# Kernel tuning notes

Measured on AMD Instinct MI355X. Metric: run time of the kernel, lower is better.

## Reference

```python
import jax, jax.numpy as jnp
import numpy as np

N, E, NREL = 50000, 800000, 4
IN, EMB, HID, OUT, LVL = 32, 32, 32, 32, 3


def setup_inputs() -> dict:
    key = jax.random.key(0)
    ks = jax.random.split(key, 24)
    f32 = jnp.float32
    inp = {
        'x': jax.random.normal(ks[0], (N, IN), f32),
        'node_feat': jax.random.normal(ks[1], (N, EMB), f32),
        'edge_feat': jax.random.normal(ks[2], (E, EMB), f32),
        'src': jax.random.randint(ks[3], (E,), 0, N, jnp.int32),
        'dst': jax.random.randint(ks[4], (E,), 0, N, jnp.int32),
        'eid': jax.random.randint(ks[5], (E,), 0, NREL, jnp.int32),
        # layer 1 (in_feat=IN)
        'Wr1': jax.random.normal(ks[6], (NREL, IN + 2 * EMB, HID), f32) * 0.1,
        'attn_w1': jax.random.normal(ks[7], (EMB + HID, 1), f32) * 0.1,
        'loop_w1': jax.random.normal(ks[8], (EMB, HID), f32) * 0.1,
        'h_bias1': jax.random.normal(ks[9], (HID,), f32) * 0.1,
        'amrm_W1': jax.random.normal(ks[10], (LVL, HID, HID), f32) * 0.1,
        'amrm_b1': jax.random.normal(ks[11], (LVL, HID), f32) * 0.1,
        'amrm_a1': jax.random.normal(ks[12], (HID, 1), f32) * 0.1,
        # layer 2 (in_feat=HID)
        'Wr2': jax.random.normal(ks[13], (NREL, HID + 2 * EMB, OUT), f32) * 0.1,
        'attn_w2': jax.random.normal(ks[14], (EMB + OUT, 1), f32) * 0.1,
        'loop_w2': jax.random.normal(ks[15], (EMB, OUT), f32) * 0.1,
        'h_bias2': jax.random.normal(ks[16], (OUT,), f32) * 0.1,
        'amrm_W2': jax.random.normal(ks[17], (LVL, OUT, OUT), f32) * 0.1,
        'amrm_b2': jax.random.normal(ks[18], (LVL, OUT), f32) * 0.1,
        'amrm_a2': jax.random.normal(ks[19], (OUT, 1), f32) * 0.1,
    }
    return inp


def _rp_layer(feat, node_feat, src, dst, eid, edge_feat,
              Wr, attn_w, loop_w, h_bias, amrm_W, amrm_b, amrm_a):
    n = node_feat.shape[0]
    ones_e = jnp.ones((src.shape[0],), feat.dtype)
    # symmetric-ish degree norm: feat scaled by out-degree^-1/2
    deg_out = jnp.clip(jax.ops.segment_sum(ones_e, src, num_segments=n), 1.0)
    feat = feat * (deg_out ** -0.5)[:, None]
    # per-edge gather + relation-typed linear (grouped GEMM over NREL types)
    xe = jnp.concatenate([feat[src], edge_feat, node_feat[dst]], axis=1)  # [E, in+2*emb]
    m = jnp.zeros((xe.shape[0], Wr.shape[2]), feat.dtype)
    for r in range(Wr.shape[0]):
        m = m + jnp.where((eid == r)[:, None], xe @ Wr[r], 0.0)
    # edge attention + segment softmax over incoming edges per dst node
    z = jax.nn.leaky_relu(jnp.concatenate([node_feat[dst], m], axis=1) @ attn_w)  # [E,1]
    zmax = jax.ops.segment_max(z, dst, num_segments=n)
    ez = jnp.exp(z - zmax[dst])
    a = ez / jax.ops.segment_sum(ez, dst, num_segments=n)[dst]
    # scatter-sum aggregation
    h = jax.ops.segment_sum(a * m, dst, num_segments=n)
    h = h + node_feat @ loop_w
    deg_in = jnp.clip(jax.ops.segment_sum(ones_e, dst, num_segments=n), 1.0)
    h = h * (deg_in ** -0.5)[:, None] + h_bias
    # adaptive multi-level relation module
    lv = jax.nn.relu(jnp.einsum('nh,lho->nlo', h, amrm_W) + amrm_b[None])  # [N,L,O]
    sc = jax.nn.softmax(jnp.einsum('nlo,o->nl', lv, amrm_a[:, 0]), axis=-1)  # [N,L]
    return jnp.einsum('nl,nlo->no', sc, lv)


def reference(x, node_feat, edge_feat, src, dst, eid,
              Wr1, attn_w1, loop_w1, h_bias1, amrm_W1, amrm_b1, amrm_a1,
              Wr2, attn_w2, loop_w2, h_bias2, amrm_W2, amrm_b2, amrm_a2):
    h = jax.nn.relu(_rp_layer(x, node_feat, src, dst, eid, edge_feat,
                              Wr1, attn_w1, loop_w1, h_bias1, amrm_W1, amrm_b1, amrm_a1))
    h = jax.nn.relu(_rp_layer(h, node_feat, src, dst, eid, edge_feat,
                              Wr2, attn_w2, loop_w2, h_bias2, amrm_W2, amrm_b2, amrm_a2))
    return h
```

## Files before the change

### kernel.cpp

```cpp
#include <hip/hip_runtime.h>

#define NN 50000
#define NE 800000

#define O_DEGIN   0
#define O_DEGOUT  50048
#define O_ROWPTR  100096
#define O_CURSOR  150208
#define O_EINFO   200256
#define O_FEATN   1800256
#define O_ZF      3400256
#define O_ZNRD    3600320
#define O_VV      3800384
#define O_EZ      3800832
#define O_NFT     4600832
#define O_WDENT   6200832
#define O_YACC    6450880
#define O_H1      19250880
#define O_WT      20850880


__global__ __launch_bounds__(256) void k_deg(const int* __restrict__ src,
                                             const int* __restrict__ dst,
                                             int* degin, int* degout) {
    int e = blockIdx.x * 256 + threadIdx.x;
    if (e < NE) {
        atomicAdd(&degin[dst[e]], 1);
        atomicAdd(&degout[src[e]], 1);
    }
}

__global__ __launch_bounds__(1024) void k_scan(const int* __restrict__ degin,
                                               int* rowptr, int* cursor) {
    __shared__ int swsum[16];
    __shared__ int stot;
    int t = threadIdx.x;
    int lane = t & 63, w = t >> 6;
    int carry = 0;
    for (int ch = 0; ch < 4; ch++) {
        int base = ch * 16384 + t * 16;
        int v[16];
        int s = 0;
#pragma unroll
        for (int j = 0; j < 16; j++) {
            v[j] = (base + j < NN) ? degin[base + j] : 0;
            s += v[j];
        }
        int incl = s;
#pragma unroll
        for (int off = 1; off < 64; off <<= 1) {
            int x = __shfl_up(incl, off, 64);
            if (lane >= off) incl += x;
        }
        if (lane == 63) swsum[w] = incl;
        __syncthreads();
        if (w == 0) {
            int y = (lane < 16) ? swsum[lane] : 0;
            int yi = y;
#pragma unroll
            for (int off = 1; off < 16; off <<= 1) {
                int x = __shfl_up(yi, off, 64);
                if (lane >= off) yi += x;
            }
            if (lane < 16) swsum[lane] = yi - y;
            if (lane == 15) stot = yi;
        }
        __syncthreads();
        int excl = carry + swsum[w] + (incl - s);
#pragma unroll
        for (int j = 0; j < 16; j++) {
            if (base + j < NN) { rowptr[base + j] = excl; cursor[base + j] = excl; }
            excl += v[j];
        }
        carry += stot;
        __syncthreads();
    }
    if (t == 0) rowptr[NN] = carry;
}

__global__ __launch_bounds__(256) void k_scatter(const int* __restrict__ src,
                                                 const int* __restrict__ dst,
                                                 const int* __restrict__ eid,
                                                 int* cursor, int2* einfo) {
    int e = blockIdx.x * 256 + threadIdx.x;
    if (e >= NE) return;
    int slot = atomicAdd(&cursor[dst[e]], 1);
    einfo[slot] = make_int2(src[e] | (eid[e] << 20), e);
}


__global__ __launch_bounds__(384) void k_prevec(const float* __restrict__ Wr,
                                                const float* __restrict__ attw,
                                                float* __restrict__ vvec) {
    int t = threadIdx.x;
    int r = (t >> 5) & 3, k = t & 31, part = t >> 7;
    int row = (part == 0) ? (32 + k) : (part == 1) ? k : (64 + k);
    const float* wrow = Wr + (size_t)r * 3072 + row * 32;
    float s = 0.f;
#pragma unroll
    for (int c = 0; c < 32; c++) s += wrow[c] * attw[32 + c];
    vvec[t] = s;
}

__global__ __launch_bounds__(512) void k_wt(const float* __restrict__ Wr,
                                            const float* __restrict__ lw,
                                            const float* __restrict__ aW,
                                            float* __restrict__ WT) {
    int tid = threadIdx.x;
    int mat = tid >> 5, i = tid & 31;
    const float* srcb;
    if (mat < 4)        srcb = Wr + (size_t)mat * 3072 + i;
    else if (mat < 8)   srcb = Wr + (size_t)(mat - 4) * 3072 + 1024 + i;
    else if (mat < 12)  srcb = Wr + (size_t)(mat - 8) * 3072 + 2048 + i;
    else if (mat == 12) srcb = lw + i;
    else                srcb = aW + (size_t)(mat - 13) * 1024 + i;
    float* d = WT + (size_t)mat * 1024 + (size_t)i * 4;
#pragma unroll
    for (int c = 0; c < 32; c++)
        d[(c >> 2) * 128 + (c & 3)] = srcb[(size_t)c * 32];
}

__global__ __launch_bounds__(128) void k_nodeproj(const float* __restrict__ feat,
                                                  const float* __restrict__ nfeat,
                                                  const float* __restrict__ attw,
                                                  const float* __restrict__ vvec,
                                                  const int* __restrict__ degout,
                                                  float* __restrict__ featn,
                                                  float* __restrict__ nfT,
                                                  float* __restrict__ zF,
                                                  float* __restrict__ znrd) {
    int n = blockIdx.x * 128 + threadIdx.x;
    if (n >= NN) return;
    int dg = degout[n];
    float sc0 = rsqrtf((float)(dg > 1 ? dg : 1));
    const float* fin = feat + (size_t)n * 32;
    const float* nin = nfeat + (size_t)n * 32;
    float fv[32], nv[32];
#pragma unroll
    for (int k = 0; k < 32; k += 4) {
        float4 f4 = *(const float4*)&fin[k];
        fv[k] = f4.x * sc0; fv[k + 1] = f4.y * sc0;
        fv[k + 2] = f4.z * sc0; fv[k + 3] = f4.w * sc0;
        float4 n4 = *(const float4*)&nin[k];
        nv[k] = n4.x; nv[k + 1] = n4.y; nv[k + 2] = n4.z; nv[k + 3] = n4.w;
    }
    float* fo = featn + (size_t)n * 32;
#pragma unroll
    for (int k = 0; k < 32; k += 4)
        *(float4*)&fo[k] = make_float4(fv[k], fv[k + 1], fv[k + 2], fv[k + 3]);
#pragma unroll
    for (int k = 0; k < 32; k++) nfT[(size_t)k * NN + n] = nv[k];
    float zn = 0.f;
#pragma unroll
    for (int k = 0; k < 32; k++) zn += nv[k] * attw[k];
#pragma unroll
    for (int r = 0; r < 4; r++) {
        float zf = 0.f, zd = 0.f;
        const float* vf = vvec + 128 + r * 32;
        const float* vd = vvec + 256 + r * 32;
#pragma unroll
        for (int k = 0; k < 32; k++) { zf += fv[k] * vf[k]; zd += nv[k] * vd[k]; }
        zF[r * NN + n] = zf;
        znrd[r * NN + n] = zn + zd;
    }
}

__global__ __launch_bounds__(256) void k_ez(const int* __restrict__ src,
                                            const int* __restrict__ dst,
                                            const int* __restrict__ eid,
                                            const float* __restrict__ efeat,
                                            const float* __restrict__ zF,
                                            const float* __restrict__ znrd,
                                            const float* __restrict__ vvec,
                                            float* __restrict__ ez) {
    int e = blockIdx.x * 256 + threadIdx.x;
    int s = src[e], d = dst[e], r = eid[e];
    const float* er = efeat + (size_t)e * 32;
    float d0 = 0.f, d1 = 0.f, d2 = 0.f, d3 = 0.f;
#pragma unroll
    for (int k = 0; k < 32; k += 4) {
        float4 f = *(const float4*)&er[k];
        d0 += f.x * vvec[k]       + f.y * vvec[k + 1]
            + f.z * vvec[k + 2]   + f.w * vvec[k + 3];
        d1 += f.x * vvec[32 + k]  + f.y * vvec[33 + k]
            + f.z * vvec[34 + k]  + f.w * vvec[35 + k];
        d2 += f.x * vvec[64 + k]  + f.y * vvec[65 + k]
            + f.z * vvec[66 + k]  + f.w * vvec[67 + k];
        d3 += f.x * vvec[96 + k]  + f.y * vvec[97 + k]
            + f.z * vvec[98 + k]  + f.w * vvec[99 + k];
    }
    float dot = (r == 0) ? d0 : (r == 1) ? d1 : (r == 2) ? d2 : d3;
    float z = znrd[r * NN + d] + zF[r * NN + s] + dot;
    z = z > 0.f ? z : 0.01f * z;
    ez[e] = __expf(z);
}

__global__ __launch_bounds__(512) void k_agg(const int* __restrict__ rowptr,
                                             const int2* __restrict__ einfo,
                                             const float* __restrict__ ez,
                                             const float* __restrict__ efeat,
                                             const float* __restrict__ featn,
                                             float* __restrict__ yacc,
                                             float* __restrict__ wdenT) {
    int tid = threadIdx.x;
    int lane = tid & 63;
    int wid = tid >> 6;
    int n0 = blockIdx.x * 8;
    int n = n0 + wid;
    int c = lane & 31;
    int p = lane >> 5;

    int rp0 = rowptr[n];
    int deg = rowptr[n + 1] - rp0;

    float yf0 = 0.f, yf1 = 0.f, yf2 = 0.f, yf3 = 0.f;
    float ye0 = 0.f, ye1 = 0.f, ye2 = 0.f, ye3 = 0.f;
    float w0 = 0.f, w1 = 0.f, w2 = 0.f, w3 = 0.f, den = 0.f;

    int2 meA = make_int2(0, 0), meB = make_int2(0, 0);
    float ezA = 0.f, efA = 0.f, fnA = 0.f;
    if (p < deg) {
        meA = einfo[rp0 + p];
        ezA = ez[meA.y];
        efA = efeat[(size_t)meA.y * 32 + c];
        fnA = featn[(size_t)(meA.x & 0xFFFFF) * 32 + c];
    }
    if (p + 2 < deg) meB = einfo[rp0 + p + 2];

    for (int t = p; t < deg; t += 2) {
        float ezB = 0.f, efB = 0.f, fnB = 0.f;
        int2 meC = make_int2(0, 0);
        if (t + 2 < deg) {
            ezB = ez[meB.y];
            efB = efeat[(size_t)meB.y * 32 + c];
            fnB = featn[(size_t)(meB.x & 0xFFFFF) * 32 + c];
        }
        if (t + 4 < deg) meC = einfo[rp0 + t + 4];
        int rb = meA.x >> 20;
        float e0 = (rb == 0) ? ezA : 0.f;
        float e1 = (rb == 1) ? ezA : 0.f;
        float e2 = (rb == 2) ? ezA : 0.f;
        float e3 = (rb == 3) ? ezA : 0.f;
        yf0 += e0 * fnA; yf1 += e1 * fnA; yf2 += e2 * fnA; yf3 += e3 * fnA;
        ye0 += e0 * efA; ye1 += e1 * efA; ye2 += e2 * efA; ye3 += e3 * efA;
        w0 += e0; w1 += e1; w2 += e2; w3 += e3;
        den += ezA;
        meA = meB; ezA = ezB; efA = efB; fnA = fnB; meB = meC;
    }

    yf0 += __shfl_xor(yf0, 32); yf1 += __shfl_xor(yf1, 32);
    yf2 += __shfl_xor(yf2, 32); yf3 += __shfl_xor(yf3, 32);
    ye0 += __shfl_xor(ye0, 32); ye1 += __shfl_xor(ye1, 32);
    ye2 += __shfl_xor(ye2, 32); ye3 += __shfl_xor(ye3, 32);
    w0 += __shfl_xor(w0, 32); w1 += __shfl_xor(w1, 32);
    w2 += __shfl_xor(w2, 32); w3 += __shfl_xor(w3, 32);
    den += __shfl_xor(den, 32);

    if (lane < 5) {
        float wv = (lane == 0) ? w0 : (lane == 1) ? w1 : (lane == 2) ? w2
                 : (lane == 3) ? w3 : den;
        wdenT[lane * NN + n] = wv;
    }

    float* yr = yacc + (size_t)n * 256 + p * 128 + c;
    yr[0]  = p ? ye0 : yf0;
    yr[32] = p ? ye1 : yf1;
    yr[64] = p ? ye2 : yf2;
    yr[96] = p ? ye3 : yf3;
}

__global__ __launch_bounds__(256) void k_postAB(const int* __restrict__ rowptr,
                                                const float* __restrict__ yacc,
                                                const float* __restrict__ wdenT,
                                                const float* __restrict__ nfeat,
                                                const float* __restrict__ WT,
                                                const float* __restrict__ hbias,
                                                const float* __restrict__ ab,
                                                const float* __restrict__ aa,
                                                float* __restrict__ out) {
    __shared__ alignas(16) float sy[8 * 256];
    __shared__ alignas(16) float snf[8 * 32];
    __shared__ float sh[8 * 32];
    int tid = threadIdx.x;
    int n0 = blockIdx.x * 8;

    {
        const float4* ys = (const float4*)(yacc + (size_t)n0 * 256);
        float4* yd = (float4*)sy;
        yd[tid] = ys[tid];
        yd[tid + 256] = ys[tid + 256];
        snf[tid] = nfeat[(size_t)n0 * 32 + tid];
    }
    __syncthreads();

    int lane = tid & 63;
    int wid = tid >> 6;
    int g = lane >> 5, i = lane & 31;
    int node = wid * 2 + g;
    int n = n0 + node;
    int deg = rowptr[n + 1] - rowptr[n];
    const float* row = sy + node * 256;
    const float* nv = snf + node * 32;
    const float* Wt = WT + (size_t)i * 4;

    float h = 0.f;
#pragma unroll 2
    for (int pr = 0; pr < 8; pr++) {
        const float* W = Wt + pr * 1024;
        const float* rw = row + pr * 32;
        float t = 0.f;
#pragma unroll
        for (int c = 0; c < 32; c += 4) {
            float4 wv = *(const float4*)&W[c * 32];
            float4 v  = *(const float4*)&rw[c];
            t += v.x * wv.x + v.y * wv.y + v.z * wv.z + v.w * wv.w;
        }
        h += t;
    }
#pragma unroll 1
    for (int r = 0; r < 4; r++) {
        float wr = wdenT[(size_t)r * NN + n];
        const float* W = Wt + (8 + r) * 1024;
        float t = 0.f;
#pragma unroll
        for (int c = 0; c < 32; c += 4) {
            float4 wv = *(const float4*)&W[c * 32];
            float4 v  = *(const float4*)&nv[c];
            t += v.x * wv.x + v.y * wv.y + v.z * wv.z + v.w * wv.w;
        }
        h += wr * t;
    }
    float den = wdenT[(size_t)4 * NN + n];
    h *= (deg > 0) ? 1.f / den : 0.f;
    {
        const float* W = Wt + 12 * 1024;
        float t = 0.f;
#pragma unroll
        for (int c = 0; c < 32; c += 4) {
            float4 wv = *(const float4*)&W[c * 32];
            float4 v  = *(const float4*)&nv[c];
            t += v.x * wv.x + v.y * wv.y + v.z * wv.z + v.w * wv.w;
        }
        h += t;
    }
    float hsc = rsqrtf((float)(deg > 1 ? deg : 1));
    h = h * hsc + hbias[i];
    sh[node * 32 + i] = h;

    const float* hn = sh + node * 32;
    float a0 = ab[i], a1 = ab[32 + i], a2 = ab[64 + i];
#pragma unroll 2
    for (int c = 0; c < 32; c += 4) {
        float4 v  = *(const float4*)&hn[c];
        float4 w0 = *(const float4*)&Wt[13 * 1024 + c * 32];
        float4 w1 = *(const float4*)&Wt[14 * 1024 + c * 32];
        float4 w2 = *(const float4*)&Wt[15 * 1024 + c * 32];
        a0 += v.x * w0.x + v.y * w0.y + v.z * w0.z + v.w * w0.w;
        a1 += v.x * w1.x + v.y * w1.y + v.z * w1.z + v.w * w1.w;
        a2 += v.x * w2.x + v.y * w2.y + v.z * w2.z + v.w * w2.w;
    }
    float lv0 = a0 > 0.f ? a0 : 0.f;
    float lv1 = a1 > 0.f ? a1 : 0.f;
    float lv2 = a2 > 0.f ? a2 : 0.f;
    float aai = aa[i];
    float s0 = lv0 * aai, s1 = lv1 * aai, s2 = lv2 * aai;
#pragma unroll
    for (int off = 16; off >= 1; off >>= 1) {
        s0 += __shfl_xor(s0, off);
        s1 += __shfl_xor(s1, off);
        s2 += __shfl_xor(s2, off);
    }
    float mx = fmaxf(s0, fmaxf(s1, s2));
    float e0 = __expf(s0 - mx), e1 = __expf(s1 - mx), e2 = __expf(s2 - mx);
    float inv = 1.f / (e0 + e1 + e2);
    float o = (e0 * lv0 + e1 * lv1 + e2 * lv2) * inv;
    out[(size_t)n * 32 + i] = fmaxf(o, 0.f);
}


static void launch_layer(const float* feat, const float* nf, const float* efeat,
                         const int* src, const int* dst, const int* eid,
                         const float* Wr, const float* attw, const float* lw,
                         const float* hb, const float* aW, const float* ab,
                         const float* aa, float* wsf, int* wsi, float* out,
                         hipStream_t stream) {
    k_prevec<<<1, 384, 0, stream>>>(Wr, attw, wsf + O_VV);
    k_wt<<<1, 512, 0, stream>>>(Wr, lw, aW, wsf + O_WT);
    k_nodeproj<<<391, 128, 0, stream>>>(feat, nf, attw, wsf + O_VV, wsi + O_DEGOUT,
                                        wsf + O_FEATN, wsf + O_NFT,
                                        wsf + O_ZF, wsf + O_ZNRD);
    k_ez<<<3125, 256, 0, stream>>>(src, dst, eid, efeat, wsf + O_ZF, wsf + O_ZNRD,
                                   wsf + O_VV, wsf + O_EZ);
    k_agg<<<6250, 512, 0, stream>>>(wsi + O_ROWPTR, (const int2*)(wsi + O_EINFO),
                                    wsf + O_EZ, efeat, wsf + O_FEATN,
                                    wsf + O_YACC, wsf + O_WDENT);
    k_postAB<<<6250, 256, 0, stream>>>(wsi + O_ROWPTR, wsf + O_YACC, wsf + O_WDENT,
                                       nf, wsf + O_WT, hb, ab, aa, out);
}

extern "C" void kernel_launch(void* const* d_in, const int* in_sizes, int n_in,
                              void* d_out, int out_size, void* d_ws, size_t ws_size,
                              hipStream_t stream) {
    const float* x     = (const float*)d_in[0];
    const float* nfeat = (const float*)d_in[1];
    const float* efeat = (const float*)d_in[2];
    const int*   src   = (const int*)d_in[3];
    const int*   dst   = (const int*)d_in[4];
    const int*   eid   = (const int*)d_in[5];
    const float* Wr1   = (const float*)d_in[6];
    const float* attw1 = (const float*)d_in[7];
    const float* lw1   = (const float*)d_in[8];
    const float* hb1   = (const float*)d_in[9];
    const float* aW1   = (const float*)d_in[10];
    const float* ab1   = (const float*)d_in[11];
    const float* aa1   = (const float*)d_in[12];
    const float* Wr2   = (const float*)d_in[13];
    const float* attw2 = (const float*)d_in[14];
    const float* lw2   = (const float*)d_in[15];
    const float* hb2   = (const float*)d_in[16];
    const float* aW2   = (const float*)d_in[17];
    const float* ab2   = (const float*)d_in[18];
    const float* aa2   = (const float*)d_in[19];

    float* wsf = (float*)d_ws;
    int*   wsi = (int*)d_ws;
    float* out = (float*)d_out;

    hipMemsetAsync(d_ws, 0, (size_t)O_ROWPTR * 4, stream);

    k_deg<<<NE / 256, 256, 0, stream>>>(src, dst, wsi + O_DEGIN, wsi + O_DEGOUT);
    k_scan<<<1, 1024, 0, stream>>>(wsi + O_DEGIN, wsi + O_ROWPTR, wsi + O_CURSOR);
    k_scatter<<<NE / 256, 256, 0, stream>>>(src, dst, eid, wsi + O_CURSOR,
                                            (int2*)(wsi + O_EINFO));

    launch_layer(x, nfeat, efeat, src, dst, eid, Wr1, attw1, lw1, hb1, aW1, ab1, aa1,
                 wsf, wsi, wsf + O_H1, stream);
    launch_layer(wsf + O_H1, nfeat, efeat, src, dst, eid, Wr2, attw2, lw2, hb2,
                 aW2, ab2, aa2, wsf, wsi, out, stream);
}
```

Measured before the change: 737.2 us.

## Stage post-aggregation weights in LDS and process four node tiles per block

```diff
diff --git a/kernel.cpp b/kernel.cpp
--- a/kernel.cpp
+++ b/kernel.cpp
@@ -278,103 +278,124 @@
                                                 const float* __restrict__ ab,
                                                 const float* __restrict__ aa,
                                                 float* __restrict__ out) {
+    __shared__ alignas(16) float sw[13 * 1024];
     __shared__ alignas(16) float sy[8 * 256];
     __shared__ alignas(16) float snf[8 * 32];
     __shared__ float sh[8 * 32];
     int tid = threadIdx.x;
-    int n0 = blockIdx.x * 8;
+    int n00 = blockIdx.x * 32;
 
     {
-        const float4* ys = (const float4*)(yacc + (size_t)n0 * 256);
-        float4* yd = (float4*)sy;
-        yd[tid] = ys[tid];
-        yd[tid + 256] = ys[tid + 256];
-        snf[tid] = nfeat[(size_t)n0 * 32 + tid];
-    }
-    __syncthreads();
+        const float4* w4 = (const float4*)WT;
+        float4* s4 = (float4*)sw;
+        for (int j = tid; j < 3328; j += 256) s4[j] = w4[j];
+    }
 
     int lane = tid & 63;
     int wid = tid >> 6;
     int g = lane >> 5, i = lane & 31;
     int node = wid * 2 + g;
-    int n = n0 + node;
-    int deg = rowptr[n + 1] - rowptr[n];
-    const float* row = sy + node * 256;
-    const float* nv = snf + node * 32;
-    const float* Wt = WT + (size_t)i * 4;
-
-    float h = 0.f;
+    const float* Wt = sw + (size_t)i * 4;
+    const float* At = WT + (size_t)i * 4;
+    float hb = hbias[i];
+    float ab0 = ab[i], ab1 = ab[32 + i], ab2 = ab[64 + i];
+    float aai = aa[i];
+
+    for (int b = 0; b < 4; b++) {
+        int nb0 = n00 + b * 8;
+        __syncthreads();
+        {
+            const float4* ys = (const float4*)yacc;
+            float4* yd = (float4*)sy;
+            size_t gb = (size_t)nb0 * 64;
+            size_t lim = (size_t)NN * 64;
+            size_t i0 = gb + tid, i1 = gb + 256 + tid;
+            yd[tid]       = (i0 < lim) ? ys[i0] : make_float4(0.f, 0.f, 0.f, 0.f);
+            yd[tid + 256] = (i1 < lim) ? ys[i1] : make_float4(0.f, 0.f, 0.f, 0.f);
+            int nfi = nb0 * 32 + tid;
+            snf[tid] = (nfi < NN * 32) ? nfeat[nfi] : 0.f;
+        }
+        __syncthreads();
+
+        int n = nb0 + node;
+        if (n < NN) {
+            int deg = rowptr[n + 1] - rowptr[n];
+            const float* row = sy + node * 256;
+            const float* nv = snf + node * 32;
+
+            float h = 0.f;
 #pragma unroll 2
-    for (int pr = 0; pr < 8; pr++) {
-        const float* W = Wt + pr * 1024;
-        const float* rw = row + pr * 32;
-        float t = 0.f;
-#pragma unroll
-        for (int c = 0; c < 32; c += 4) {
-            float4 wv = *(const float4*)&W[c * 32];
-            float4 v  = *(const float4*)&rw[c];
-            t += v.x * wv.x + v.y * wv.y + v.z * wv.z + v.w * wv.w;
-        }
-        h += t;
-    }
-#pragma unroll 1
-    for (int r = 0; r < 4; r++) {
-        float wr = wdenT[(size_t)r * NN + n];
-        const float* W = Wt + (8 + r) * 1024;
-        float t = 0.f;
-#pragma unroll
-        for (int c = 0; c < 32; c += 4) {
-            float4 wv = *(const float4*)&W[c * 32];
-            float4 v  = *(const float4*)&nv[c];
-            t += v.x * wv.x + v.y * wv.y + v.z * wv.z + v.w * wv.w;
-        }
-        h += wr * t;
-    }
-    float den = wdenT[(size_t)4 * NN + n];
-    h *= (deg > 0) ? 1.f / den : 0.f;
-    {
-        const float* W = Wt + 12 * 1024;
-        float t = 0.f;
-#pragma unroll
-        for (int c = 0; c < 32; c += 4) {
-            float4 wv = *(const float4*)&W[c * 32];
-            float4 v  = *(const float4*)&nv[c];
-            t += v.x * wv.x + v.y * wv.y + v.z * wv.z + v.w * wv.w;
-        }
-        h += t;
-    }
-    float hsc = rsqrtf((float)(deg > 1 ? deg : 1));
-    h = h * hsc + hbias[i];
-    sh[node * 32 + i] = h;
-
-    const float* hn = sh + node * 32;
-    float a0 = ab[i], a1 = ab[32 + i], a2 = ab[64 + i];
+            for (int pr = 0; pr < 8; pr++) {
+                const float* W = Wt + pr * 1024;
+                const float* rw = row + pr * 32;
+                float t = 0.f;
+#pragma unroll
+                for (int c = 0; c < 32; c += 4) {
+                    float4 wv = *(const float4*)&W[c * 32];
+                    float4 v  = *(const float4*)&rw[c];
+                    t += v.x * wv.x + v.y * wv.y + v.z * wv.z + v.w * wv.w;
+                }
+                h += t;
+            }
+#pragma unroll
+            for (int r = 0; r < 4; r++) {
+                float wr = wdenT[(size_t)r * NN + n];
+                const float* W = Wt + (8 + r) * 1024;
+                float t = 0.f;
+#pragma unroll
+                for (int c = 0; c < 32; c += 4) {
+                    float4 wv = *(const float4*)&W[c * 32];
+                    float4 v  = *(const float4*)&nv[c];
+                    t += v.x * wv.x + v.y * wv.y + v.z * wv.z + v.w * wv.w;
+                }
+                h += wr * t;
+            }
+            float den = wdenT[(size_t)4 * NN + n];
+            h *= (deg > 0) ? 1.f / den : 0.f;
+            {
+                const float* W = Wt + 12 * 1024;
+                float t = 0.f;
+#pragma unroll
+                for (int c = 0; c < 32; c += 4) {
+                    float4 wv = *(const float4*)&W[c * 32];
+                    float4 v  = *(const float4*)&nv[c];
+                    t += v.x * wv.x + v.y * wv.y + v.z * wv.z + v.w * wv.w;
+                }
+                h += t;
+            }
+            float hsc = rsqrtf((float)(deg > 1 ? deg : 1));
+            h = h * hsc + hb;
+            sh[node * 32 + i] = h;
+
+            const float* hn = sh + node * 32;
+            float a0 = ab0, a1 = ab1, a2 = ab2;
 #pragma unroll 2
-    for (int c = 0; c < 32; c += 4) {
-        float4 v  = *(const float4*)&hn[c];
-        float4 w0 = *(const float4*)&Wt[13 * 1024 + c * 32];
-        float4 w1 = *(const float4*)&Wt[14 * 1024 + c * 32];
-        float4 w2 = *(const float4*)&Wt[15 * 1024 + c * 32];
-        a0 += v.x * w0.x + v.y * w0.y + v.z * w0.z + v.w * w0.w;
-        a1 += v.x * w1.x + v.y * w1.y + v.z * w1.z + v.w * w1.w;
-        a2 += v.x * w2.x + v.y * w2.y + v.z * w2.z + v.w * w2.w;
-    }
-    float lv0 = a0 > 0.f ? a0 : 0.f;
-    float lv1 = a1 > 0.f ? a1 : 0.f;
-    float lv2 = a2 > 0.f ? a2 : 0.f;
-    float aai = aa[i];
-    float s0 = lv0 * aai, s1 = lv1 * aai, s2 = lv2 * aai;
-#pragma unroll
-    for (int off = 16; off >= 1; off >>= 1) {
-        s0 += __shfl_xor(s0, off);
-        s1 += __shfl_xor(s1, off);
-        s2 += __shfl_xor(s2, off);
-    }
-    float mx = fmaxf(s0, fmaxf(s1, s2));
-    float e0 = __expf(s0 - mx), e1 = __expf(s1 - mx), e2 = __expf(s2 - mx);
-    float inv = 1.f / (e0 + e1 + e2);
-    float o = (e0 * lv0 + e1 * lv1 + e2 * lv2) * inv;
-    out[(size_t)n * 32 + i] = fmaxf(o, 0.f);
+            for (int c = 0; c < 32; c += 4) {
+                float4 v  = *(const float4*)&hn[c];
+                float4 w0 = *(const float4*)&At[13 * 1024 + c * 32];
+                float4 w1 = *(const float4*)&At[14 * 1024 + c * 32];
+                float4 w2 = *(const float4*)&At[15 * 1024 + c * 32];
+                a0 += v.x * w0.x + v.y * w0.y + v.z * w0.z + v.w * w0.w;
+                a1 += v.x * w1.x + v.y * w1.y + v.z * w1.z + v.w * w1.w;
+                a2 += v.x * w2.x + v.y * w2.y + v.z * w2.z + v.w * w2.w;
+            }
+            float lv0 = a0 > 0.f ? a0 : 0.f;
+            float lv1 = a1 > 0.f ? a1 : 0.f;
+            float lv2 = a2 > 0.f ? a2 : 0.f;
+            float s0 = lv0 * aai, s1 = lv1 * aai, s2 = lv2 * aai;
+#pragma unroll
+            for (int off = 16; off >= 1; off >>= 1) {
+                s0 += __shfl_xor(s0, off);
+                s1 += __shfl_xor(s1, off);
+                s2 += __shfl_xor(s2, off);
+            }
+            float mx = fmaxf(s0, fmaxf(s1, s2));
+            float e0 = __expf(s0 - mx), e1 = __expf(s1 - mx), e2 = __expf(s2 - mx);
+            float inv = 1.f / (e0 + e1 + e2);
+            float o = (e0 * lv0 + e1 * lv1 + e2 * lv2) * inv;
+            out[(size_t)n * 32 + i] = fmaxf(o, 0.f);
+        }
+    }
 }
 
 
@@ -394,7 +415,7 @@
     k_agg<<<6250, 512, 0, stream>>>(wsi + O_ROWPTR, (const int2*)(wsi + O_EINFO),
                                     wsf + O_EZ, efeat, wsf + O_FEATN,
                                     wsf + O_YACC, wsf + O_WDENT);
-    k_postAB<<<6250, 256, 0, stream>>>(wsi + O_ROWPTR, wsf + O_YACC, wsf + O_WDENT,
+    k_postAB<<<1563, 256, 0, stream>>>(wsi + O_ROWPTR, wsf + O_YACC, wsf + O_WDENT,
                                        nf, wsf + O_WT, hb, ab, aa, out);
 }
 
```

New measurement: 736.9 us. No clear change (-0.0%).
